# Optimization experiments

Hardware: AMD Instinct MI355X
Metric: run time of the kernel (lower is better)

## Reference

```python
import jax, jax.numpy as jnp
import numpy as np

IMAGE_SIZE = 1024
BATCH = 16


def _make_grid(n):
    # matches torch buffer: meshgrid('xy') over linspace(-1,1,n), stacked last -> [n, n, 2]
    r = np.linspace(-1.0, 1.0, num=n)
    gx, gy = np.meshgrid(r, r, indexing='xy')
    return jnp.asarray(np.stack([gx, gy], axis=-1).astype(np.float32))


def setup_inputs() -> dict:
    key = jax.random.key(0)
    k1, k2 = jax.random.split(key)
    saliency_map = jax.random.uniform(k1, (BATCH, IMAGE_SIZE, IMAGE_SIZE), dtype=jnp.float32)
    ior_glimpse_hist_mask = jnp.ones((BATCH, 1, IMAGE_SIZE, IMAGE_SIZE), dtype=jnp.float32)
    current_location = jax.random.uniform(k2, (BATCH, 2), dtype=jnp.float32, minval=-0.9, maxval=0.9)
    grid = _make_grid(IMAGE_SIZE)
    return {"saliency_map": saliency_map, "ior_glimpse_hist_mask": ior_glimpse_hist_mask,
            "current_location": current_location, "grid": grid}


def reference(saliency_map, ior_glimpse_hist_mask, current_location, grid):
    # soft_ior=True, ior_mask_size=None, glimpse_size_to_mask_size_ratio=1
    B = saliency_map.shape[0]
    N = grid.shape[0]
    sal = saliency_map[:, None]                       # [B,1,N,N]
    grid_flat = grid.reshape(-1, 2)                   # [N*N,2]

    # ImageLocationMasker(current_location, custom_mask_size=1)
    radius = (1.0 ** 2) / (N ** 2) / 2.0
    cur_dist = jnp.mean(jnp.square(grid_flat[None] - current_location[:, None]), axis=-1)  # [B,N*N]
    cur_mask = (cur_dist <= radius).reshape(B, 1, N, N)
    sal = jnp.where(cur_mask, 0.0, sal)

    hist = ior_glimpse_hist_mask
    # soft_ior: if hist is all zeros, replace with ones
    hist = jnp.where(jnp.all(hist == 0.0), jnp.ones_like(hist), hist)

    masked = hist * sal                                # [B,1,N,N]

    grid_chw = jnp.transpose(grid, (2, 0, 1))[None]    # [1,2,N,N]
    neg_inf = jnp.float32(-jnp.inf)
    mg = jnp.where(masked > 0.0, grid_chw, neg_inf)    # [B,2,N,N]
    max_sal = jnp.max(masked.reshape(B, -1), axis=-1)  # [B]
    mg = jnp.where(masked >= max_sal[:, None, None, None], mg, neg_inf)

    d = jnp.mean(jnp.square(mg.reshape(B, 2, -1).transpose(0, 2, 1) - current_location[:, None]), axis=-1)  # [B,N*N]
    idx = jnp.argmin(d, axis=-1)                       # [B]
    py = idx // N
    px = idx % N

    loc = jnp.stack([px + 1, py + 1], axis=-1).astype(jnp.float32)  # flip(-1) then +1
    loc = 2.0 * (loc / N) - 1.0                        # [B,2]

    all_zero = jnp.all(masked.reshape(B, -1) == 0.0, axis=-1)[:, None]
    next_xy_location = jnp.where(all_zero, jnp.ones_like(loc), loc)

    # per-sample eps from gathered saliency value at the chosen pixel
    sm_value = sal[jnp.arange(B), 0, py, px]
    sm_value = jnp.maximum(sm_value, 1e-4)
    eps = (10.0 / sm_value)[:, None, None]             # [B,1,1]

    rbf_arg = jnp.mean(jnp.square(grid[None] - loc[:, None, None]), axis=-1)  # [B,N,N]
    mask = jnp.exp(-jnp.square(rbf_arg * eps))[:, None]                        # [B,1,N,N]

    hist = jnp.clip(hist * (1.0 - mask), 0.0, 1.0)
    return next_xy_location, hist, mask
```

## Files before the change

kernel.cpp:

```cpp
#include <hip/hip_runtime.h>
#include <math.h>

#define NN 1024
#define NPIX (NN * NN)
#define NB 16
#define BPB 128
#define NBLK (NB * BPB)
#define ROWS 8
#define RADIUS 4.76837158203125e-07f

struct Partial {
    float m1, d1; int i1;
    float m2, d2; int i2;
    unsigned flags;
    int pad;
};

__device__ __forceinline__ void comp_upd(float om, float od, int oi,
                                         float& bm, float& bd, int& bi) {
    if (om > bm || (om == bm && (od < bd || (od == bd && oi < bi)))) {
        bm = om; bd = od; bi = oi;
    }
}

__global__ __launch_bounds__(256) void k_reduce(
        const float* __restrict__ sal, const float* __restrict__ hist,
        const float* __restrict__ cur, const float* __restrict__ grid,
        Partial* __restrict__ part) {
    __shared__ float r[NN];
    __shared__ Partial sp[4];
    const int tid = threadIdx.x;
    for (int i = tid; i < NN; i += 256) r[i] = grid[i * 2];
    const int b   = blockIdx.x >> 7;
    const int blk = blockIdx.x & (BPB - 1);
    const float cx = cur[b * 2 + 0];
    const float cy = cur[b * 2 + 1];
    __syncthreads();

    float hdx2[4];
    #pragma unroll
    for (int j = 0; j < 4; ++j) {
        const float dx = r[tid * 4 + j] - cx;
        hdx2[j] = 0.5f * (dx * dx);
    }
    float hdy2[ROWS];
    #pragma unroll
    for (int it = 0; it < ROWS; ++it) {
        const float dy = r[blk * ROWS + it] - cy;
        hdy2[it] = 0.5f * (dy * dy);
    }

    const size_t base = (size_t)b * NPIX + (size_t)blk * (ROWS * NN) + (size_t)tid * 4;
    float bm1 = -INFINITY, bd1 = INFINITY; int bi1 = 0;
    float bm2 = -INFINITY, bd2 = INFINITY; int bi2 = 0;
    float ah = 0.0f, am1 = 0.0f, am2 = 0.0f;

    #pragma unroll
    for (int it = 0; it < ROWS; ++it) {
        const float4 s4 = *(const float4*)(sal + base + it * NN);
        const float4 h4 = *(const float4*)(hist + base + it * NN);
        const int p0 = blk * (ROWS * NN) + it * NN + tid * 4;
        #pragma unroll
        for (int j = 0; j < 4; ++j) {
            const float sv = ((const float*)&s4)[j];
            const float hv = ((const float*)&h4)[j];
            const float cd = hdx2[j] + hdy2[it];
            const float salv = (cd <= RADIUS) ? 0.0f : sv;
            const float m1v = hv * salv;
            ah  = fmaxf(ah,  fabsf(hv));
            am1 = fmaxf(am1, fabsf(m1v));
            am2 = fmaxf(am2, fabsf(salv));
            if (m1v > bm1 || (m1v == bm1 && cd < bd1)) { bm1 = m1v; bd1 = cd; bi1 = p0 + j; }
            if (salv > bm2 || (salv == bm2 && cd < bd2)) { bm2 = salv; bd2 = cd; bi2 = p0 + j; }
        }
    }

    unsigned fl = (ah > 0.0f ? 1u : 0u) | (am1 > 0.0f ? 2u : 0u) | (am2 > 0.0f ? 4u : 0u);

    #pragma unroll
    for (int s = 32; s; s >>= 1) {
        float om = __shfl_xor(bm1, s); float od = __shfl_xor(bd1, s); int oi = __shfl_xor(bi1, s);
        comp_upd(om, od, oi, bm1, bd1, bi1);
        om = __shfl_xor(bm2, s); od = __shfl_xor(bd2, s); oi = __shfl_xor(bi2, s);
        comp_upd(om, od, oi, bm2, bd2, bi2);
        fl |= __shfl_xor(fl, s);
    }
    const int wave = tid >> 6;
    const int lane = tid & 63;
    if (lane == 0) {
        Partial P; P.m1 = bm1; P.d1 = bd1; P.i1 = bi1;
        P.m2 = bm2; P.d2 = bd2; P.i2 = bi2; P.flags = fl; P.pad = 0;
        sp[wave] = P;
    }
    __syncthreads();
    if (tid == 0) {
        Partial P = sp[0];
        for (int w = 1; w < 4; ++w) {
            const Partial Q = sp[w];
            comp_upd(Q.m1, Q.d1, Q.i1, P.m1, P.d1, P.i1);
            comp_upd(Q.m2, Q.d2, Q.i2, P.m2, P.d2, P.i2);
            P.flags |= Q.flags;
        }
        part[blockIdx.x] = P;
    }
}

__global__ __launch_bounds__(1024) void k_final(
        const Partial* __restrict__ part, const float* __restrict__ sal,
        const float* __restrict__ cur, const float* __restrict__ grid,
        float* __restrict__ out_xy, float* __restrict__ params) {
    __shared__ unsigned shf[16];
    unsigned f = 0;
    for (int i = threadIdx.x; i < NBLK; i += 1024) f |= part[i].flags;
    #pragma unroll
    for (int s = 32; s; s >>= 1) f |= __shfl_xor(f, s);
    const int wave = threadIdx.x >> 6;
    const int lane = threadIdx.x & 63;
    if (lane == 0) shf[wave] = f;
    __syncthreads();
    unsigned allf = 0;
    #pragma unroll
    for (int w = 0; w < 16; ++w) allf |= shf[w];
    const bool histnz = (allf & 1u) != 0;

    const int b = wave;
    float bm = -INFINITY, bd = INFINITY; int bi = 0x7fffffff;
    unsigned anz = 0;
    #pragma unroll
    for (int k = 0; k < 2; ++k) {
        const Partial Q = part[b * BPB + k * 64 + lane];
        const float m = histnz ? Q.m1 : Q.m2;
        const float d = histnz ? Q.d1 : Q.d2;
        const int   i = histnz ? Q.i1 : Q.i2;
        anz |= histnz ? (Q.flags & 2u) : (Q.flags & 4u);
        comp_upd(m, d, i, bm, bd, bi);
    }
    #pragma unroll
    for (int s = 32; s; s >>= 1) {
        const float om = __shfl_xor(bm, s);
        const float od = __shfl_xor(bd, s);
        const int   oi = __shfl_xor(bi, s);
        anz |= __shfl_xor(anz, s);
        comp_upd(om, od, oi, bm, bd, bi);
    }
    if (lane == 0) {
        const bool all_zero = (anz == 0u);
        const int idx = (bm > 0.0f) ? bi : 0;
        const int py = idx >> 10;
        const int px = idx & (NN - 1);
        const float lx = 2.0f * ((float)(px + 1) / 1024.0f) - 1.0f;
        const float ly = 2.0f * ((float)(py + 1) / 1024.0f) - 1.0f;
        const float gx = grid[px * 2];
        const float gy = grid[py * 2];
        const float cx = cur[b * 2 + 0];
        const float cy = cur[b * 2 + 1];
        const float dx = gx - cx;
        const float dy = gy - cy;
        const float hdx2 = 0.5f * (dx * dx);
        const float hdy2 = 0.5f * (dy * dy);
        const float cd = hdx2 + hdy2;
        const float sv = sal[(size_t)b * NPIX + idx];
        const float salv = (cd <= RADIUS) ? 0.0f : sv;
        const float sm = fmaxf(salv, 0.0001f);
        const float eps = 10.0f / sm;
        out_xy[2 * b + 0] = all_zero ? 1.0f : lx;
        out_xy[2 * b + 1] = all_zero ? 1.0f : ly;
        params[4 * b + 0] = lx;
        params[4 * b + 1] = ly;
        params[4 * b + 2] = eps;
        params[4 * b + 3] = histnz ? 0.0f : 1.0f;
    }
}

__global__ __launch_bounds__(256) void k_apply(
        const float* __restrict__ hist, const float* __restrict__ grid,
        const float* __restrict__ params, float* __restrict__ out_hist,
        float* __restrict__ out_mask) {
    __shared__ float r[NN];
    const int tid = threadIdx.x;
    for (int i = tid; i < NN; i += 256) r[i] = grid[i * 2];
    const int b   = blockIdx.x >> 7;
    const int blk = blockIdx.x & (BPB - 1);
    const float lx  = params[4 * b + 0];
    const float ly  = params[4 * b + 1];
    const float eps = params[4 * b + 2];
    const bool useones = params[4 * b + 3] != 0.0f;
    __syncthreads();

    float hdx2[4];
    #pragma unroll
    for (int j = 0; j < 4; ++j) {
        const float dx = r[tid * 4 + j] - lx;
        hdx2[j] = 0.5f * (dx * dx);
    }

    const size_t base = (size_t)b * NPIX + (size_t)blk * (ROWS * NN) + (size_t)tid * 4;
    #pragma unroll
    for (int it = 0; it < ROWS; ++it) {
        const float dy = r[blk * ROWS + it] - ly;
        const float hdy2 = 0.5f * (dy * dy);
        const float4 h4 = *(const float4*)(hist + base + it * NN);
        float4 m4, o4;
        #pragma unroll
        for (int j = 0; j < 4; ++j) {
            const float rbf = hdx2[j] + hdy2;
            const float t = rbf * eps;
            const float mk = __expf(-(t * t));
            const float hv = useones ? 1.0f : ((const float*)&h4)[j];
            float ho = hv * (1.0f - mk);
            ho = fminf(fmaxf(ho, 0.0f), 1.0f);
            ((float*)&m4)[j] = mk;
            ((float*)&o4)[j] = ho;
        }
        *(float4*)(out_mask + base + it * NN) = m4;
        *(float4*)(out_hist + base + it * NN) = o4;
    }
}

extern "C" void kernel_launch(void* const* d_in, const int* in_sizes, int n_in,
                              void* d_out, int out_size, void* d_ws, size_t ws_size,
                              hipStream_t stream) {
    const float* sal  = (const float*)d_in[0];
    const float* hist = (const float*)d_in[1];
    const float* cur  = (const float*)d_in[2];
    const float* grid = (const float*)d_in[3];

    float* out      = (float*)d_out;
    float* out_xy   = out;
    float* out_hist = out + NB * 2;
    float* out_mask = out_hist + NB * NPIX;

    Partial* part = (Partial*)d_ws;
    float* params = (float*)((char*)d_ws + NBLK * sizeof(Partial));

    k_reduce<<<NBLK, 256, 0, stream>>>(sal, hist, cur, grid, part);
    k_final<<<1, 1024, 0, stream>>>(part, sal, cur, grid, out_xy, params);
    k_apply<<<NBLK, 256, 0, stream>>>(hist, grid, params, out_hist, out_mask);
}
```

Before: 257.6 us.

## Fuse final reduction into reduce kernel via last-block atomic counter; nontemporal IO

The separate single-block final kernel is folded into the reduce kernel. Each block bumps an atomic counter after writing its partial, and the last block to finish does the cross-batch final reduction with 4 waves handling 4 batches each. This removes one kernel launch and its gap, at the cost of a memset of the counter and a serialized tail done by one block. The saliency loads and both output stores are also made nontemporal, to keep streaming data from displacing hist in cache.

```diff
diff --git a/kernel.cpp b/kernel.cpp
--- a/kernel.cpp
+++ b/kernel.cpp
@@ -9,6 +9,8 @@
 #define ROWS 8
 #define RADIUS 4.76837158203125e-07f
 
+typedef float f4 __attribute__((ext_vector_type(4)));
+
 struct Partial {
     float m1, d1; int i1;
     float m2, d2; int i2;
@@ -23,12 +25,15 @@
     }
 }
 
-__global__ __launch_bounds__(256) void k_reduce(
+__global__ __launch_bounds__(256) void k_reduce_final(
         const float* __restrict__ sal, const float* __restrict__ hist,
         const float* __restrict__ cur, const float* __restrict__ grid,
-        Partial* __restrict__ part) {
+        Partial* __restrict__ part, unsigned* __restrict__ cnt,
+        float* __restrict__ out_xy, float* __restrict__ params) {
     __shared__ float r[NN];
     __shared__ Partial sp[4];
+    __shared__ int sLast;
+    __shared__ unsigned sfl[4];
     const int tid = threadIdx.x;
     for (int i = tid; i < NN; i += 256) r[i] = grid[i * 2];
     const int b   = blockIdx.x >> 7;
@@ -57,13 +62,13 @@
 
     #pragma unroll
     for (int it = 0; it < ROWS; ++it) {
-        const float4 s4 = *(const float4*)(sal + base + it * NN);
-        const float4 h4 = *(const float4*)(hist + base + it * NN);
+        const f4 s4 = __builtin_nontemporal_load((const f4*)(sal + base + it * NN));
+        const f4 h4 = *(const f4*)(hist + base + it * NN);
         const int p0 = blk * (ROWS * NN) + it * NN + tid * 4;
         #pragma unroll
         for (int j = 0; j < 4; ++j) {
-            const float sv = ((const float*)&s4)[j];
-            const float hv = ((const float*)&h4)[j];
+            const float sv = s4[j];
+            const float hv = h4[j];
             const float cd = hdx2[j] + hdy2[it];
             const float salv = (cd <= RADIUS) ? 0.0f : sv;
             const float m1v = hv * salv;
@@ -102,73 +107,67 @@
             P.flags |= Q.flags;
         }
         part[blockIdx.x] = P;
-    }
-}
-
-__global__ __launch_bounds__(1024) void k_final(
-        const Partial* __restrict__ part, const float* __restrict__ sal,
-        const float* __restrict__ cur, const float* __restrict__ grid,
-        float* __restrict__ out_xy, float* __restrict__ params) {
-    __shared__ unsigned shf[16];
+        __threadfence();
+        const unsigned old = atomicAdd(cnt, 1u);
+        sLast = (old == NBLK - 1) ? 1 : 0;
+    }
+    __syncthreads();
+    if (!sLast) return;
+
+    __threadfence();
     unsigned f = 0;
-    for (int i = threadIdx.x; i < NBLK; i += 1024) f |= part[i].flags;
+    for (int i = tid; i < NBLK; i += 256) f |= part[i].flags;
     #pragma unroll
     for (int s = 32; s; s >>= 1) f |= __shfl_xor(f, s);
-    const int wave = threadIdx.x >> 6;
-    const int lane = threadIdx.x & 63;
-    if (lane == 0) shf[wave] = f;
-    __syncthreads();
-    unsigned allf = 0;
-    #pragma unroll
-    for (int w = 0; w < 16; ++w) allf |= shf[w];
+    if (lane == 0) sfl[wave] = f;
+    __syncthreads();
+    const unsigned allf = sfl[0] | sfl[1] | sfl[2] | sfl[3];
     const bool histnz = (allf & 1u) != 0;
 
-    const int b = wave;
-    float bm = -INFINITY, bd = INFINITY; int bi = 0x7fffffff;
-    unsigned anz = 0;
-    #pragma unroll
-    for (int k = 0; k < 2; ++k) {
-        const Partial Q = part[b * BPB + k * 64 + lane];
-        const float m = histnz ? Q.m1 : Q.m2;
-        const float d = histnz ? Q.d1 : Q.d2;
-        const int   i = histnz ? Q.i1 : Q.i2;
-        anz |= histnz ? (Q.flags & 2u) : (Q.flags & 4u);
-        comp_upd(m, d, i, bm, bd, bi);
-    }
-    #pragma unroll
-    for (int s = 32; s; s >>= 1) {
-        const float om = __shfl_xor(bm, s);
-        const float od = __shfl_xor(bd, s);
-        const int   oi = __shfl_xor(bi, s);
-        anz |= __shfl_xor(anz, s);
-        comp_upd(om, od, oi, bm, bd, bi);
-    }
-    if (lane == 0) {
-        const bool all_zero = (anz == 0u);
-        const int idx = (bm > 0.0f) ? bi : 0;
-        const int py = idx >> 10;
-        const int px = idx & (NN - 1);
-        const float lx = 2.0f * ((float)(px + 1) / 1024.0f) - 1.0f;
-        const float ly = 2.0f * ((float)(py + 1) / 1024.0f) - 1.0f;
-        const float gx = grid[px * 2];
-        const float gy = grid[py * 2];
-        const float cx = cur[b * 2 + 0];
-        const float cy = cur[b * 2 + 1];
-        const float dx = gx - cx;
-        const float dy = gy - cy;
-        const float hdx2 = 0.5f * (dx * dx);
-        const float hdy2 = 0.5f * (dy * dy);
-        const float cd = hdx2 + hdy2;
-        const float sv = sal[(size_t)b * NPIX + idx];
-        const float salv = (cd <= RADIUS) ? 0.0f : sv;
-        const float sm = fmaxf(salv, 0.0001f);
-        const float eps = 10.0f / sm;
-        out_xy[2 * b + 0] = all_zero ? 1.0f : lx;
-        out_xy[2 * b + 1] = all_zero ? 1.0f : ly;
-        params[4 * b + 0] = lx;
-        params[4 * b + 1] = ly;
-        params[4 * b + 2] = eps;
-        params[4 * b + 3] = histnz ? 0.0f : 1.0f;
+    for (int bb = 0; bb < 4; ++bb) {
+        const int fb = wave * 4 + bb;
+        float bm = -INFINITY, bd = INFINITY; int bi = 0x7fffffff;
+        unsigned anz = 0;
+        #pragma unroll
+        for (int k = 0; k < 2; ++k) {
+            const Partial Q = part[fb * BPB + k * 64 + lane];
+            const float m = histnz ? Q.m1 : Q.m2;
+            const float d = histnz ? Q.d1 : Q.d2;
+            const int   i = histnz ? Q.i1 : Q.i2;
+            anz |= histnz ? (Q.flags & 2u) : (Q.flags & 4u);
+            comp_upd(m, d, i, bm, bd, bi);
+        }
+        #pragma unroll
+        for (int s = 32; s; s >>= 1) {
+            const float om = __shfl_xor(bm, s);
+            const float od = __shfl_xor(bd, s);
+            const int   oi = __shfl_xor(bi, s);
+            anz |= __shfl_xor(anz, s);
+            comp_upd(om, od, oi, bm, bd, bi);
+        }
+        if (lane == 0) {
+            const bool all_zero = (anz == 0u);
+            const int idx = (bm > 0.0f) ? bi : 0;
+            const int py = idx >> 10;
+            const int px = idx & (NN - 1);
+            const float lx = 2.0f * ((float)(px + 1) / 1024.0f) - 1.0f;
+            const float ly = 2.0f * ((float)(py + 1) / 1024.0f) - 1.0f;
+            const float fcx = cur[fb * 2 + 0];
+            const float fcy = cur[fb * 2 + 1];
+            const float dx = r[px] - fcx;
+            const float dy = r[py] - fcy;
+            const float cd = 0.5f * (dx * dx) + 0.5f * (dy * dy);
+            const float sv = sal[(size_t)fb * NPIX + idx];
+            const float salv = (cd <= RADIUS) ? 0.0f : sv;
+            const float sm = fmaxf(salv, 0.0001f);
+            const float eps = 10.0f / sm;
+            out_xy[2 * fb + 0] = all_zero ? 1.0f : lx;
+            out_xy[2 * fb + 1] = all_zero ? 1.0f : ly;
+            params[4 * fb + 0] = lx;
+            params[4 * fb + 1] = ly;
+            params[4 * fb + 2] = eps;
+            params[4 * fb + 3] = histnz ? 0.0f : 1.0f;
+        }
     }
 }
 
@@ -199,21 +198,21 @@
     for (int it = 0; it < ROWS; ++it) {
         const float dy = r[blk * ROWS + it] - ly;
         const float hdy2 = 0.5f * (dy * dy);
-        const float4 h4 = *(const float4*)(hist + base + it * NN);
-        float4 m4, o4;
+        const f4 h4 = *(const f4*)(hist + base + it * NN);
+        f4 m4, o4;
         #pragma unroll
         for (int j = 0; j < 4; ++j) {
             const float rbf = hdx2[j] + hdy2;
             const float t = rbf * eps;
             const float mk = __expf(-(t * t));
-            const float hv = useones ? 1.0f : ((const float*)&h4)[j];
+            const float hv = useones ? 1.0f : h4[j];
             float ho = hv * (1.0f - mk);
             ho = fminf(fmaxf(ho, 0.0f), 1.0f);
-            ((float*)&m4)[j] = mk;
-            ((float*)&o4)[j] = ho;
-        }
-        *(float4*)(out_mask + base + it * NN) = m4;
-        *(float4*)(out_hist + base + it * NN) = o4;
+            m4[j] = mk;
+            o4[j] = ho;
+        }
+        __builtin_nontemporal_store(m4, (f4*)(out_mask + base + it * NN));
+        __builtin_nontemporal_store(o4, (f4*)(out_hist + base + it * NN));
     }
 }
 
@@ -230,10 +229,11 @@
     float* out_hist = out + NB * 2;
     float* out_mask = out_hist + NB * NPIX;
 
-    Partial* part = (Partial*)d_ws;
-    float* params = (float*)((char*)d_ws + NBLK * sizeof(Partial));
-
-    k_reduce<<<NBLK, 256, 0, stream>>>(sal, hist, cur, grid, part);
-    k_final<<<1, 1024, 0, stream>>>(part, sal, cur, grid, out_xy, params);
+    Partial*  part   = (Partial*)d_ws;
+    unsigned* cnt    = (unsigned*)((char*)d_ws + NBLK * sizeof(Partial));
+    float*    params = (float*)((char*)d_ws + NBLK * sizeof(Partial) + 256);
+
+    (void)hipMemsetAsync(cnt, 0, sizeof(unsigned), stream);
+    k_reduce_final<<<NBLK, 256, 0, stream>>>(sal, hist, cur, grid, part, cnt, out_xy, params);
     k_apply<<<NBLK, 256, 0, stream>>>(hist, grid, params, out_hist, out_mask);
 }
```

Result: slower. 307.1 us (+19.2%).
